# Optimization experiments

Hardware: AMD Instinct MI355X
Metric: run time of the kernel (lower is better)

## Reference

```python
import jax, jax.numpy as jnp
import numpy as np

B, S, D, H, DK, DV, DFF = 8, 1024, 512, 8, 64, 64, 2048
EPS = 1e-6
NEG = -1e10


def _ln(x, w, b):
    # LayerNorm over last two dims ([S, D]) as in nn.LayerNorm([seq_len, d_model])
    m = jnp.mean(x, axis=(-2, -1), keepdims=True)
    v = jnp.var(x, axis=(-2, -1), keepdims=True)
    return (x - m) / jnp.sqrt(v + EPS) * w + b


def _mha(q, k, v, wq, bq, wk, bk, wv, bv, wo, bo, mask):
    # batched version of the per-head loop: wq/wk [H, D, DK], wv [H, D, DV]
    qh = jnp.einsum('bsd,hdk->bhsk', q, wq) + bq[:, None, :]
    kh = jnp.einsum('bsd,hdk->bhsk', k, wk) + bk[:, None, :]
    vh = jnp.einsum('bsd,hdv->bhsv', v, wv) + bv[:, None, :]
    sc = jnp.einsum('bhqk,bhmk->bhqm', qh, kh) / jnp.asarray(np.sqrt(DK), jnp.float32)
    sc = jnp.where(mask[:, None, None, :] == 0, NEG, sc)  # mask over key dim
    a = jax.nn.softmax(sc, axis=-1)
    o = jnp.einsum('bhqm,bhmv->bhqv', a, vh)
    o = o.transpose(0, 2, 1, 3).reshape(q.shape[0], q.shape[1], H * DV)
    return o @ wo.T + bo


def setup_inputs() -> dict:
    key = jax.random.key(0)
    ks = jax.random.split(key, 24)

    def w(k, shape):
        return (jax.random.normal(k, shape, jnp.float32) * 0.02)

    inp = {
        'x': jax.random.normal(ks[0], (B, S, D), jnp.float32),
        'y': jax.random.normal(ks[1], (B, S, D), jnp.float32),
        'src_mask': jax.random.randint(ks[2], (B, S), 0, 2, jnp.int32),
        'trg_mask': jax.random.randint(ks[3], (B, S), 0, 2, jnp.int32),
    }
    i = 4
    for pre in ('m1', 'm2'):
        inp[pre + '_wq'] = w(ks[i], (H, D, DK)); i += 1
        inp[pre + '_bq'] = jnp.zeros((H, DK), jnp.float32)
        inp[pre + '_wk'] = w(ks[i], (H, D, DK)); i += 1
        inp[pre + '_bk'] = jnp.zeros((H, DK), jnp.float32)
        inp[pre + '_wv'] = w(ks[i], (H, D, DV)); i += 1
        inp[pre + '_bv'] = jnp.zeros((H, DV), jnp.float32)
        inp[pre + '_wo'] = w(ks[i], (D, H * DV)); i += 1
        inp[pre + '_bo'] = jnp.zeros((D,), jnp.float32)
    inp['pw1'] = w(ks[i], (DFF, D)); i += 1
    inp['pb1'] = jnp.zeros((DFF,), jnp.float32)
    inp['pw2'] = w(ks[i], (D, DFF)); i += 1
    inp['pb2'] = jnp.zeros((D,), jnp.float32)
    for n in ('ln1', 'ln2', 'ln3'):
        inp[n + '_w'] = jnp.ones((S, D), jnp.float32)
        inp[n + '_b'] = jnp.zeros((S, D), jnp.float32)
    return inp


def reference(x, y, src_mask, trg_mask,
              m1_wq, m1_bq, m1_wk, m1_bk, m1_wv, m1_bv, m1_wo, m1_bo,
              m2_wq, m2_bq, m2_wk, m2_bk, m2_wv, m2_bv, m2_wo, m2_bo,
              pw1, pb1, pw2, pb2,
              ln1_w, ln1_b, ln2_w, ln2_b, ln3_w, ln3_b):
    # self-attention + residual + LN (dropout is identity at eval)
    h = _mha(x, x, x, m1_wq, m1_bq, m1_wk, m1_bk, m1_wv, m1_bv, m1_wo, m1_bo, trg_mask)
    x1 = _ln(x + h, ln1_w, ln1_b)
    # cross-attention
    h = _mha(x1, y, y, m2_wq, m2_bq, m2_wk, m2_bk, m2_wv, m2_bv, m2_wo, m2_bo, src_mask)
    x2 = _ln(x1 + h, ln2_w, ln2_b)
    # position-wise FFN
    ff = jax.nn.relu(x2 @ pw1.T + pb1) @ pw2.T + pb2
    return _ln(x2 + ff, ln3_w, ln3_b)
```

## Files before the change

### kernel.cpp

```cpp
#include <hip/hip_runtime.h>
#include <hip/hip_bf16.h>

#define B_   8
#define S_   1024
#define D_   512
#define H_   8
#define DK_  64
#define DFF_ 2048

typedef __hip_bfloat16 bf16;
typedef __attribute__((ext_vector_type(8))) short bf16x8;
typedef __attribute__((ext_vector_type(4))) float f32x4;

__device__ __forceinline__ float ldmix(const void* p, size_t i, int f) {
    return f ? __bfloat162float(((const bf16*)p)[i]) : ((const float*)p)[i];
}
__device__ __forceinline__ void store_o(float* p, float v) { *p = v; }
__device__ __forceinline__ void store_o(bf16* p, float v)  { *p = __float2bfloat16(v); }

__device__ __forceinline__ void gl_lds16(const void* g, void* l) {
    __builtin_amdgcn_global_load_lds(
        (const __attribute__((address_space(1))) unsigned int*)g,
        (__attribute__((address_space(3))) unsigned int*)l, 16, 0, 0);
}

#define WAITV(N)  asm volatile("s_waitcnt vmcnt(" #N ")" ::: "memory")
#define WAITLGKM0 asm volatile("s_waitcnt lgkmcnt(0)" ::: "memory")

__global__ __launch_bounds__(64) void detect_k(const unsigned short* __restrict__ x,
                                               float* __restrict__ stats,
                                               int* __restrict__ flag)
{
    if (threadIdx.x < 48) stats[threadIdx.x] = 0.f;
    int cnt = 0;
    for (int i = threadIdx.x; i < 4096; i += 64) {
        int e = (x[i] >> 7) & 0xFF;
        if (e >= 0xC0) cnt++;
    }
#pragma unroll
    for (int off = 32; off; off >>= 1) cnt += __shfl_xor(cnt, off);
    if (threadIdx.x == 0) { flag[0] = (cnt > 16) ? 0 : 1; flag[1] = 1; }
}

__global__ __launch_bounds__(256) void maskf_k(const int* __restrict__ trg,
                                               const int* __restrict__ src,
                                               float* __restrict__ trgf,
                                               float* __restrict__ srcf)
{
    int i = blockIdx.x * 256 + threadIdx.x;
    if (i < 8192) trgf[i] = trg[i] ? 0.f : -1.0e10f;
    else          srcf[i - 8192] = src[i - 8192] ? 0.f : -1.0e10f;
}

__global__ __launch_bounds__(256) void convxy_k(const void* __restrict__ x,
                                                const void* __restrict__ y,
                                                bf16* __restrict__ xb, bf16* __restrict__ yb,
                                                const int* __restrict__ flag)
{
    const int f = flag[0];
    const int N8 = 8192 * 512 / 8;
    int i = blockIdx.x * 256 + threadIdx.x;
    const void* src; bf16* dst; size_t base;
    if (i < N8) { src = x; dst = xb; base = (size_t)i * 8; }
    else        { src = y; dst = yb; base = (size_t)(i - N8) * 8; }
    if (f) {
        *(uint4*)(dst + base) = *(const uint4*)((const bf16*)src + base);
    } else {
        const float4 a = *(const float4*)((const float*)src + base);
        const float4 b = *(const float4*)((const float*)src + base + 4);
        bf16 o[8] = {__float2bfloat16(a.x), __float2bfloat16(a.y),
                     __float2bfloat16(a.z), __float2bfloat16(a.w),
                     __float2bfloat16(b.x), __float2bfloat16(b.y),
                     __float2bfloat16(b.z), __float2bfloat16(b.w)};
        *(uint4*)(dst + base) = *(uint4*)o;
    }
}

__global__ __launch_bounds__(256) void repack6_k(const void* __restrict__ w0, const void* __restrict__ w1,
                                                 const void* __restrict__ w2, const void* __restrict__ w3,
                                                 const void* __restrict__ w4, const void* __restrict__ w5,
                                                 bf16* __restrict__ out, const int* __restrict__ flag)
{
    const int f = flag[0];
    const int widx = blockIdx.x >> 10;
    const int j = ((blockIdx.x & 1023) << 8) + threadIdx.x;
    const void* in = widx == 0 ? w0 : widx == 1 ? w1 : widx == 2 ? w2
                   : widx == 3 ? w3 : widx == 4 ? w4 : w5;
    int n = j >> 9, d = j & 511;
    int h = n >> 6, k = n & 63;
    out[(size_t)widx * 262144 + j] =
        __float2bfloat16(ldmix(in, (size_t)h * (D_ * DK_) + (size_t)d * DK_ + k, f));
}

__global__ __launch_bounds__(256) void convw4_k(const void* __restrict__ wo1, const void* __restrict__ wo2,
                                                const void* __restrict__ pw1, const void* __restrict__ pw2,
                                                bf16* __restrict__ out, const int* __restrict__ flag)
{
    const int f = flag[0];
    const size_t i8 = (size_t)(blockIdx.x * 256 + threadIdx.x) * 8;
    const void* in; size_t off;
    if (i8 < 262144)       { in = wo1; off = 0; }
    else if (i8 < 524288)  { in = wo2; off = 262144; }
    else if (i8 < 1572864) { in = pw1; off = 524288; }
    else                   { in = pw2; off = 1572864; }
    const size_t s = i8 - off;
    if (f) {
        *(uint4*)(out + i8) = *(const uint4*)((const bf16*)in + s);
    } else {
        const float4 a = *(const float4*)((const float*)in + s);
        const float4 b = *(const float4*)((const float*)in + s + 4);
        bf16 o[8] = {__float2bfloat16(a.x), __float2bfloat16(a.y),
                     __float2bfloat16(a.z), __float2bfloat16(a.w),
                     __float2bfloat16(b.x), __float2bfloat16(b.y),
                     __float2bfloat16(b.z), __float2bfloat16(b.w)};
        *(uint4*)(out + i8) = *(uint4*)o;
    }
}

__device__ __forceinline__ void gemm_core(const bf16* __restrict__ A, const bf16* __restrict__ Wt,
                                          int K, int m0, int n0, bf16* As, bf16* Bs,
                                          f32x4 (&acc)[2][2])
{
    constexpr int NBUF = 3;
    const int tid = threadIdx.x;
    const int lane = tid & 63, w = tid >> 6;
    const int wr = w >> 1, wc = w & 1;
    const int l16 = lane & 15, quad = lane >> 4;
    const int r0 = tid >> 2;
    const int g0 = (tid & 3) ^ ((r0 >> 1) & 3);
    const bf16* pa = A  + (size_t)(m0 + r0) * K + g0 * 8;
    const bf16* pb = Wt + (size_t)(n0 + r0) * K + g0 * 8;

    int aoff[2], boff[2];
#pragma unroll
    for (int i = 0; i < 2; ++i) {
        const int ra = wr * 32 + i * 16 + l16;
        aoff[i] = ra * 32 + (quad ^ ((ra >> 1) & 3)) * 8;
    }
#pragma unroll
    for (int j = 0; j < 2; ++j) {
        const int rb = wc * 32 + j * 16 + l16;
        boff[j] = rb * 32 + (quad ^ ((rb >> 1) & 3)) * 8;
    }

    auto stage = [&](int bi, int k0) {
        gl_lds16(pa + k0, As + bi * 2048 + w * 512);
        gl_lds16(pb + k0, Bs + bi * 2048 + w * 512);
    };

    const int NT = K >> 5;
    stage(0, 0);
    stage(1, 32);
    int cur = 0, nxt = 2;

    for (int t = 0; t < NT; ++t) {
        if (t + 2 < NT) {
            stage(nxt, (t + 2) << 5);
            WAITV(4);
        } else if (t + 1 < NT) {
            WAITV(2);
        } else {
            WAITV(0);
        }
        __builtin_amdgcn_s_barrier();
        __builtin_amdgcn_sched_barrier(0);

        const bf16* Ab = As + cur * 2048;
        const bf16* Bb = Bs + cur * 2048;
        bf16x8 af[2], bg[2];
#pragma unroll
        for (int i = 0; i < 2; ++i) af[i] = *(const bf16x8*)&Ab[aoff[i]];
#pragma unroll
        for (int j = 0; j < 2; ++j) bg[j] = *(const bf16x8*)&Bb[boff[j]];
#pragma unroll
        for (int i = 0; i < 2; ++i)
#pragma unroll
            for (int j = 0; j < 2; ++j)
                acc[i][j] = __builtin_amdgcn_mfma_f32_16x16x32_bf16(af[i], bg[j], acc[i][j], 0, 0, 0);

        WAITLGKM0;
        __builtin_amdgcn_sched_barrier(0);
        __builtin_amdgcn_s_barrier();
        cur = (cur + 1 == NBUF) ? 0 : cur + 1;
        nxt = (nxt + 1 == NBUF) ? 0 : nxt + 1;
    }
}

template <bool HAS_RES, bool RELU, bool STATS, typename OutT>
__global__ __launch_bounds__(256)
void mgemm_k(const bf16* __restrict__ A, const bf16* __restrict__ Wt,
             const void* __restrict__ bias, const void* __restrict__ res,
             OutT* __restrict__ C, int N, int K, int Gx,
             const int* __restrict__ bflag, const int* __restrict__ rflag,
             float* __restrict__ stats)
{
    __shared__ bf16 As[3 * 2048];
    __shared__ bf16 Bs[3 * 2048];
    const int lin = blockIdx.x;
    const int mt = (lin & 7) * 16 + (lin >> 3) / Gx;
    const int nt = (lin >> 3) % Gx;
    const int m0 = mt * 64, n0 = nt * 64;

    f32x4 acc[2][2];
#pragma unroll
    for (int i = 0; i < 2; ++i)
#pragma unroll
        for (int j = 0; j < 2; ++j) acc[i][j] = (f32x4){0.f, 0.f, 0.f, 0.f};

    gemm_core(A, Wt, K, m0, n0, As, Bs, acc);

    const int tid = threadIdx.x;
    const int lane = tid & 63, w = tid >> 6;
    const int wr = w >> 1, wc = w & 1;
    const int l16 = lane & 15, quad = lane >> 4;
    const int bf = bflag[0];
    int rf = 0;
    if constexpr (HAS_RES) rf = rflag[0];

    float s = 0.f, s2 = 0.f;
#pragma unroll
    for (int i = 0; i < 2; ++i) {
        const int row = m0 + wr * 32 + i * 16 + quad * 4;
#pragma unroll
        for (int j = 0; j < 2; ++j) {
            const int col = n0 + wc * 32 + j * 16 + l16;
            const float bv = ldmix(bias, col, bf);
#pragma unroll
            for (int r = 0; r < 4; ++r) {
                float c = acc[i][j][r] + bv;
                if constexpr (RELU) c = fmaxf(c, 0.f);
                if constexpr (HAS_RES) c += ldmix(res, (size_t)(row + r) * N + col, rf);
                if constexpr (STATS) { s += c; s2 += c * c; }
                store_o(&C[(size_t)(row + r) * N + col], c);
            }
        }
    }
    if constexpr (STATS) {
#pragma unroll
        for (int off = 32; off; off >>= 1) { s += __shfl_xor(s, off); s2 += __shfl_xor(s2, off); }
        __syncthreads();
        float* red = (float*)As;
        if (lane == 0) { red[w * 2] = s; red[w * 2 + 1] = s2; }
        __syncthreads();
        if (tid == 0) {
            const int b = m0 >> 10;
            atomicAdd(&stats[b * 2],     red[0] + red[2] + red[4] + red[6]);
            atomicAdd(&stats[b * 2 + 1], red[1] + red[3] + red[5] + red[7]);
        }
    }
}

__global__ __launch_bounds__(256)
void mgemm_qkv_k(const bf16* __restrict__ A, const bf16* __restrict__ Wbase,
                 const void* __restrict__ bq, const void* __restrict__ bk, const void* __restrict__ bv,
                 bf16* __restrict__ qout, bf16* __restrict__ kout, bf16* __restrict__ vtout,
                 int Gx, int roff, const int* __restrict__ bflag)
{
    __shared__ bf16 As[3 * 2048];
    __shared__ bf16 Bs[3 * 2048];
    const int lin = blockIdx.x;
    const int mt = (lin & 7) * 16 + (lin >> 3) / Gx;
    const int nt = (lin >> 3) % Gx;
    const int m0 = mt * 64, n0 = nt * 64;

    f32x4 acc[2][2];
#pragma unroll
    for (int i = 0; i < 2; ++i)
#pragma unroll
        for (int j = 0; j < 2; ++j) acc[i][j] = (f32x4){0.f, 0.f, 0.f, 0.f};

    gemm_core(A, Wbase, 512, m0, n0, As, Bs, acc);

    const int tid = threadIdx.x;
    const int lane = tid & 63, w = tid >> 6;
    const int wr = w >> 1, wc = w & 1;
    const int l16 = lane & 15, quad = lane >> 4;
    const int bf = bflag[0];
    const int region = roff + (nt >> 3);
    const void* bptr = region == 0 ? bq : (region == 1 ? bk : bv);

#pragma unroll
    for (int i = 0; i < 2; ++i) {
        const int row = m0 + wr * 32 + i * 16 + quad * 4;
#pragma unroll
        for (int j = 0; j < 2; ++j) {
            const int col = n0 + wc * 32 + j * 16 + l16;
            const int colr = col & 511;
            const float bvv = ldmix(bptr, colr, bf);
#pragma unroll
            for (int r = 0; r < 4; ++r) {
                const int rr = row + r;
                float c = acc[i][j][r] + bvv;
                if (region == 0) {
                    qout[(size_t)rr * 512 + colr] = __float2bfloat16(c * 0.125f);
                } else if (region == 1) {
                    kout[(size_t)rr * 512 + colr] = __float2bfloat16(c);
                } else {
                    const int b = rr >> 10, key = rr & 1023;
                    vtout[((size_t)(b * 512 + colr) << 10) | key] = __float2bfloat16(c);
                }
            }
        }
    }
}

__global__ __launch_bounds__(256)
void mfattn_k(const bf16* __restrict__ Q, const bf16* __restrict__ Kb,
              const bf16* __restrict__ Vt, const float* __restrict__ maskf,
              bf16* __restrict__ O)
{
    const int lin = blockIdx.x;
    const int j = lin >> 3, xcd = lin & 7;
    const int head = xcd * 8 + (j >> 4);
    const int qt = j & 15;
    const int b = head >> 3, h = head & 7, s0 = qt * 64;
    const int tid = threadIdx.x;
    const int lane = tid & 63, w = tid >> 6;
    const int l16 = lane & 15, quad = lane >> 4;
    const int bS = b * S_, hc = h * DK_;
    const size_t vtb = (size_t)(b * H_ + h) * (DK_ * S_);

    __shared__ bf16 QPs[64 * 72];
    __shared__ bf16 Ks[64 * 72];
    __shared__ bf16 Vs[64 * 72];

    const int str = tid >> 3;
    const int stc = (tid & 7) * 8;

    *(uint4*)&QPs[str * 72 + stc]        = *(const uint4*)&Q[(size_t)(bS + s0 + str) * D_ + hc + stc];
    *(uint4*)&QPs[(str + 32) * 72 + stc] = *(const uint4*)&Q[(size_t)(bS + s0 + str + 32) * D_ + hc + stc];
    __syncthreads();

    const bf16x8 aq0 = *(const bf16x8*)&QPs[(w * 16 + l16) * 72 + quad * 8];
    const bf16x8 aq1 = *(const bf16x8*)&QPs[(w * 16 + l16) * 72 + quad * 8 + 32];

    f32x4 acc_o[4];
#pragma unroll
    for (int nb = 0; nb < 4; ++nb) acc_o[nb] = (f32x4){0.f, 0.f, 0.f, 0.f};
    float lrow[4] = {0.f, 0.f, 0.f, 0.f};

    for (int t0 = 0; t0 < S_; t0 += 64) {
        __syncthreads();
        *(uint4*)&Ks[str * 72 + stc]        = *(const uint4*)&Kb[(size_t)(bS + t0 + str) * D_ + hc + stc];
        *(uint4*)&Ks[(str + 32) * 72 + stc] = *(const uint4*)&Kb[(size_t)(bS + t0 + str + 32) * D_ + hc + stc];
        *(uint4*)&Vs[str * 72 + stc]        = *(const uint4*)&Vt[vtb + (size_t)str * S_ + t0 + stc];
        *(uint4*)&Vs[(str + 32) * 72 + stc] = *(const uint4*)&Vt[vtb + (size_t)(str + 32) * S_ + t0 + stc];
        __syncthreads();

        f32x4 sacc[4];
#pragma unroll
        for (int nb = 0; nb < 4; ++nb) sacc[nb] = (f32x4){0.f, 0.f, 0.f, 0.f};
#pragma unroll
        for (int nb = 0; nb < 4; ++nb) {
            const bf16x8 b0 = *(const bf16x8*)&Ks[(nb * 16 + l16) * 72 + quad * 8];
            const bf16x8 b1 = *(const bf16x8*)&Ks[(nb * 16 + l16) * 72 + quad * 8 + 32];
            sacc[nb] = __builtin_amdgcn_mfma_f32_16x16x32_bf16(aq0, b0, sacc[nb], 0, 0, 0);
            sacc[nb] = __builtin_amdgcn_mfma_f32_16x16x32_bf16(aq1, b1, sacc[nb], 0, 0, 0);
        }

#pragma unroll
        for (int nb = 0; nb < 4; ++nb) {
            const float mv = maskf[bS + t0 + nb * 16 + l16];
#pragma unroll
            for (int r = 0; r < 4; ++r) {
                const float p = __expf(sacc[nb][r] + mv);
                lrow[r] += p;
                QPs[(w * 16 + quad * 4 + r) * 72 + nb * 16 + l16] = __float2bfloat16(p);
            }
        }

        const bf16x8 ap0 = *(const bf16x8*)&QPs[(w * 16 + l16) * 72 + quad * 8];
        const bf16x8 ap1 = *(const bf16x8*)&QPs[(w * 16 + l16) * 72 + quad * 8 + 32];
#pragma unroll
        for (int nb = 0; nb < 4; ++nb) {
            const bf16x8 v0 = *(const bf16x8*)&Vs[(nb * 16 + l16) * 72 + quad * 8];
            const bf16x8 v1 = *(const bf16x8*)&Vs[(nb * 16 + l16) * 72 + quad * 8 + 32];
            acc_o[nb] = __builtin_amdgcn_mfma_f32_16x16x32_bf16(ap0, v0, acc_o[nb], 0, 0, 0);
            acc_o[nb] = __builtin_amdgcn_mfma_f32_16x16x32_bf16(ap1, v1, acc_o[nb], 0, 0, 0);
        }
    }

#pragma unroll
    for (int r = 0; r < 4; ++r) {
        float ls = lrow[r];
#pragma unroll
        for (int off = 8; off; off >>= 1) ls += __shfl_xor(ls, off);
        const float invl = 1.0f / ls;
        const size_t row = (size_t)(bS + s0 + w * 16 + quad * 4 + r) * D_;
#pragma unroll
        for (int nb = 0; nb < 4; ++nb)
            O[row + hc + nb * 16 + l16] = __float2bfloat16(acc_o[nb][r] * invl);
    }
}

template <bool FINAL>
__global__ __launch_bounds__(256)
void ln_apply_k(const float* __restrict__ Z, const float* __restrict__ stats,
                const void* __restrict__ w, const void* __restrict__ bb,
                bf16* __restrict__ outb, void* __restrict__ out_final,
                const int* __restrict__ flag)
{
    const int f = flag[0];
    const int b = blockIdx.y;
    const int i4 = (blockIdx.x * 256 + threadIdx.x) * 4;
    const float n = (float)(S_ * D_);
    const float m = stats[b * 2] / n;
    const float var = stats[b * 2 + 1] / n - m * m;
    const float inv = rsqrtf(var + 1e-6f);
    const size_t g = (size_t)b * (S_ * D_) + i4;
    const float4 z = *(const float4*)&Z[g];
    float v[4];
    v[0] = (z.x - m) * inv * ldmix(w, i4 + 0, f) + ldmix(bb, i4 + 0, f);
    v[1] = (z.y - m) * inv * ldmix(w, i4 + 1, f) + ldmix(bb, i4 + 1, f);
    v[2] = (z.z - m) * inv * ldmix(w, i4 + 2, f) + ldmix(bb, i4 + 2, f);
    v[3] = (z.w - m) * inv * ldmix(w, i4 + 3, f) + ldmix(bb, i4 + 3, f);
    union { ushort4 u4; unsigned short u[4]; } ov;
#pragma unroll
    for (int k = 0; k < 4; ++k) {
        bf16 t = __float2bfloat16(v[k]);
        __builtin_memcpy(&ov.u[k], &t, 2);
    }
    if constexpr (FINAL) {
        if (f) *(ushort4*)&((bf16*)out_final)[g] = ov.u4;
        else   *(float4*)&((float*)out_final)[g] = make_float4(v[0], v[1], v[2], v[3]);
    } else {
        *(ushort4*)&outb[g] = ov.u4;
    }
}

extern "C" void kernel_launch(void* const* d_in, const int* in_sizes, int n_in,
                              void* d_out, int out_size, void* d_ws, size_t ws_size,
                              hipStream_t stream)
{
    (void)in_sizes; (void)n_in; (void)out_size; (void)ws_size;

    const void* x        = d_in[0];
    const void* y        = d_in[1];
    const int*  src_mask = (const int*) d_in[2];
    const int*  trg_mask = (const int*) d_in[3];
    const void* m1_wq = d_in[4];
    const void* m1_bq = d_in[5];
    const void* m1_wk = d_in[6];
    const void* m1_bk = d_in[7];
    const void* m1_wv = d_in[8];
    const void* m1_bv = d_in[9];
    const void* m1_wo = d_in[10];
    const void* m1_bo = d_in[11];
    const void* m2_wq = d_in[12];
    const void* m2_bq = d_in[13];
    const void* m2_wk = d_in[14];
    const void* m2_bk = d_in[15];
    const void* m2_wv = d_in[16];
    const void* m2_bv = d_in[17];
    const void* m2_wo = d_in[18];
    const void* m2_bo = d_in[19];
    const void* pw1   = d_in[20];
    const void* pb1   = d_in[21];
    const void* pw2   = d_in[22];
    const void* pb2   = d_in[23];
    const void* ln1_w = d_in[24];
    const void* ln1_b = d_in[25];
    const void* ln2_w = d_in[26];
    const void* ln2_b = d_in[27];
    const void* ln3_w = d_in[28];
    const void* ln3_b = d_in[29];

    const size_t NACT = (size_t)8192 * 512;

    float* zb    = (float*)d_ws;
    float* stats = zb + NACT;
    int*   flag  = (int*)(stats + 48);
    float* trgf  = stats + 64;
    float* srcf  = trgf + 8192;
    bf16* xb16 = (bf16*)(srcf + 8192);
    bf16* yb16 = xb16 + NACT;
    bf16* qb   = yb16 + NACT;
    bf16* kb   = qb   + NACT;
    bf16* vbT  = kb   + NACT;
    bf16* aob  = vbT  + NACT;
    bf16* x1b  = aob  + NACT;
    bf16* x2b  = x1b  + NACT;
    bf16* ffb  = x2b  + NACT;
    bf16* Wq1r = ffb  + (size_t)8192 * 2048;
    bf16* Wq2r = Wq1r + 3 * 262144;
    bf16* Wo1b = Wq1r + 6 * 262144;
    bf16* Wo2b = Wo1b + 262144;
    bf16* W1b  = Wo2b + 262144;
    bf16* W2b  = W1b  + 1048576;

    detect_k<<<1, 64, 0, stream>>>((const unsigned short*)x, stats, flag);
    maskf_k<<<64, 256, 0, stream>>>(trg_mask, src_mask, trgf, srcf);
    convxy_k<<<4096, 256, 0, stream>>>(x, y, xb16, yb16, flag);
    repack6_k<<<6144, 256, 0, stream>>>(m1_wq, m1_wk, m1_wv, m2_wq, m2_wk, m2_wv, Wq1r, flag);
    convw4_k<<<1280, 256, 0, stream>>>(m1_wo, m2_wo, pw1, pw2, Wo1b, flag);

    const dim3 blk(256);
    const dim3 gln(512, B_);

    mgemm_qkv_k<<<dim3(3072), blk, 0, stream>>>(xb16, Wq1r, m1_bq, m1_bk, m1_bv, qb, kb, vbT, 24, 0, flag);
    mfattn_k<<<dim3(1024), blk, 0, stream>>>(qb, kb, vbT, trgf, aob);
    mgemm_k<true, false, true, float><<<dim3(1024), blk, 0, stream>>>(aob, Wo1b, m1_bo, x, zb, 512, 512, 8, flag, flag, stats);
    ln_apply_k<false><<<gln, blk, 0, stream>>>(zb, stats, ln1_w, ln1_b, x1b, nullptr, flag);

    mgemm_qkv_k<<<dim3(1024), blk, 0, stream>>>(x1b, Wq2r, m2_bq, m2_bk, m2_bv, qb, kb, vbT, 8, 0, flag);
    mgemm_qkv_k<<<dim3(2048), blk, 0, stream>>>(yb16, Wq2r + 262144, m2_bq, m2_bk, m2_bv, qb, kb, vbT, 16, 1, flag);
    mfattn_k<<<dim3(1024), blk, 0, stream>>>(qb, kb, vbT, srcf, aob);
    mgemm_k<true, false, true, float><<<dim3(1024), blk, 0, stream>>>(aob, Wo2b, m2_bo, x1b, zb, 512, 512, 8, flag, flag + 1, stats + 16);
    ln_apply_k<false><<<gln, blk, 0, stream>>>(zb, stats + 16, ln2_w, ln2_b, x2b, nullptr, flag);

    mgemm_k<false, true, false, bf16><<<dim3(4096), blk, 0, stream>>>(x2b, W1b, pb1, nullptr, ffb, 2048, 512, 32, flag, flag, nullptr);
    mgemm_k<true, false, true, float><<<dim3(1024), blk, 0, stream>>>(ffb, W2b, pb2, x2b, zb, 512, 2048, 8, flag, flag + 1, stats + 32);
    ln_apply_k<true><<<gln, blk, 0, stream>>>(zb, stats + 32, ln3_w, ln3_b, nullptr, d_out, flag);
}
```

Baseline: 556.7 us.

## Double the GEMM K-tile to 64 and drop the trailing barrier per iteration

The shared bf16 GEMM core now stages 64-wide K tiles (two row-halves per load) with an 8-way XOR swizzle, and issues 8 MFMAs per barrier instead of 4. The next stage is issued after the top barrier, into the buffer consumed two iterations earlier, which removes the second barrier and the lgkmcnt wait at the end of each iteration. The aim is to halve the per-K barrier and synchronisation overhead. In exchange, LDS use per block doubles to 48 KB, which may lower occupancy, and correctness relies on the three-buffer rotation ordering.

```diff
diff --git a/kernel.cpp b/kernel.cpp
--- a/kernel.cpp
+++ b/kernel.cpp
@@ -25,7 +25,6 @@
 }
 
 #define WAITV(N)  asm volatile("s_waitcnt vmcnt(" #N ")" ::: "memory")
-#define WAITLGKM0 asm volatile("s_waitcnt lgkmcnt(0)" ::: "memory")
 
 __global__ __launch_bounds__(64) void detect_k(const unsigned short* __restrict__ x,
                                                float* __restrict__ stats,
@@ -121,68 +120,67 @@
                                           int K, int m0, int n0, bf16* As, bf16* Bs,
                                           f32x4 (&acc)[2][2])
 {
-    constexpr int NBUF = 3;
     const int tid = threadIdx.x;
     const int lane = tid & 63, w = tid >> 6;
     const int wr = w >> 1, wc = w & 1;
     const int l16 = lane & 15, quad = lane >> 4;
-    const int r0 = tid >> 2;
-    const int g0 = (tid & 3) ^ ((r0 >> 1) & 3);
+    const int r0 = tid >> 3;
+    const int g0 = (tid & 7) ^ (r0 & 7);
     const bf16* pa = A  + (size_t)(m0 + r0) * K + g0 * 8;
     const bf16* pb = Wt + (size_t)(n0 + r0) * K + g0 * 8;
-
-    int aoff[2], boff[2];
+    const size_t rhalf = (size_t)32 * K;
+
+    int aoff[2][2], boff[2][2];
 #pragma unroll
     for (int i = 0; i < 2; ++i) {
         const int ra = wr * 32 + i * 16 + l16;
-        aoff[i] = ra * 32 + (quad ^ ((ra >> 1) & 3)) * 8;
-    }
-#pragma unroll
-    for (int j = 0; j < 2; ++j) {
-        const int rb = wc * 32 + j * 16 + l16;
-        boff[j] = rb * 32 + (quad ^ ((rb >> 1) & 3)) * 8;
+        const int rb = wc * 32 + i * 16 + l16;
+#pragma unroll
+        for (int ks = 0; ks < 2; ++ks) {
+            aoff[i][ks] = ra * 64 + (((ks << 2) + quad) ^ (ra & 7)) * 8;
+            boff[i][ks] = rb * 64 + (((ks << 2) + quad) ^ (rb & 7)) * 8;
+        }
     }
 
     auto stage = [&](int bi, int k0) {
-        gl_lds16(pa + k0, As + bi * 2048 + w * 512);
-        gl_lds16(pb + k0, Bs + bi * 2048 + w * 512);
+        bf16* a = As + bi * 4096;
+        bf16* b = Bs + bi * 4096;
+        gl_lds16(pa + k0,         a + w * 512);
+        gl_lds16(pa + k0 + rhalf, a + 2048 + w * 512);
+        gl_lds16(pb + k0,         b + w * 512);
+        gl_lds16(pb + k0 + rhalf, b + 2048 + w * 512);
     };
 
-    const int NT = K >> 5;
+    const int NT = K >> 6;
     stage(0, 0);
-    stage(1, 32);
-    int cur = 0, nxt = 2;
+    stage(1, 64);
+    int cur = 0;
 
     for (int t = 0; t < NT; ++t) {
-        if (t + 2 < NT) {
-            stage(nxt, (t + 2) << 5);
-            WAITV(4);
-        } else if (t + 1 < NT) {
-            WAITV(2);
-        } else {
-            WAITV(0);
-        }
+        if (t + 1 < NT) WAITV(4); else WAITV(0);
         __builtin_amdgcn_s_barrier();
         __builtin_amdgcn_sched_barrier(0);
-
-        const bf16* Ab = As + cur * 2048;
-        const bf16* Bb = Bs + cur * 2048;
-        bf16x8 af[2], bg[2];
-#pragma unroll
-        for (int i = 0; i < 2; ++i) af[i] = *(const bf16x8*)&Ab[aoff[i]];
-#pragma unroll
-        for (int j = 0; j < 2; ++j) bg[j] = *(const bf16x8*)&Bb[boff[j]];
+        if (t + 2 < NT) stage(cur == 0 ? 2 : cur - 1, (t + 2) << 6);
+
+        const bf16* Ab = As + cur * 4096;
+        const bf16* Bb = Bs + cur * 4096;
+        bf16x8 af[2][2], bg[2][2];
 #pragma unroll
         for (int i = 0; i < 2; ++i)
 #pragma unroll
-            for (int j = 0; j < 2; ++j)
-                acc[i][j] = __builtin_amdgcn_mfma_f32_16x16x32_bf16(af[i], bg[j], acc[i][j], 0, 0, 0);
-
-        WAITLGKM0;
-        __builtin_amdgcn_sched_barrier(0);
-        __builtin_amdgcn_s_barrier();
-        cur = (cur + 1 == NBUF) ? 0 : cur + 1;
-        nxt = (nxt + 1 == NBUF) ? 0 : nxt + 1;
+            for (int ks = 0; ks < 2; ++ks) {
+                af[i][ks] = *(const bf16x8*)&Ab[aoff[i][ks]];
+                bg[i][ks] = *(const bf16x8*)&Bb[boff[i][ks]];
+            }
+#pragma unroll
+        for (int ks = 0; ks < 2; ++ks)
+#pragma unroll
+            for (int i = 0; i < 2; ++i)
+#pragma unroll
+                for (int j = 0; j < 2; ++j)
+                    acc[i][j] = __builtin_amdgcn_mfma_f32_16x16x32_bf16(af[i][ks], bg[j][ks], acc[i][j], 0, 0, 0);
+
+        cur = (cur + 1 == 3) ? 0 : cur + 1;
     }
 }
 
@@ -194,8 +192,8 @@
              const int* __restrict__ bflag, const int* __restrict__ rflag,
              float* __restrict__ stats)
 {
-    __shared__ bf16 As[3 * 2048];
-    __shared__ bf16 Bs[3 * 2048];
+    __shared__ bf16 As[3 * 4096];
+    __shared__ bf16 Bs[3 * 4096];
     const int lin = blockIdx.x;
     const int mt = (lin & 7) * 16 + (lin >> 3) / Gx;
     const int nt = (lin >> 3) % Gx;
@@ -256,8 +254,8 @@
                  bf16* __restrict__ qout, bf16* __restrict__ kout, bf16* __restrict__ vtout,
                  int Gx, int roff, const int* __restrict__ bflag)
 {
-    __shared__ bf16 As[3 * 2048];
-    __shared__ bf16 Bs[3 * 2048];
+    __shared__ bf16 As[3 * 4096];
+    __shared__ bf16 Bs[3 * 4096];
     const int lin = blockIdx.x;
     const int mt = (lin & 7) * 16 + (lin >> 3) / Gx;
     const int nt = (lin >> 3) % Gx;
```

Measured after the change: 560.8 us. No clear change (+0.7%).
